# Kernel optimization log

Measured on AMD Instinct MI355X. Metric: run time of the kernel, lower is better.

## Reference

```python
import jax, jax.numpy as jnp
import numpy as np
import math

B = 200        # graphs
NPG = 512      # nodes per graph
EPG = 8192     # edges per graph (avg degree 16)
E = B * EPG
FIN = 11
H = 128


def setup_inputs() -> dict:
    key = jax.random.key(0)
    ks = jax.random.split(key, 16)
    g = jnp.arange(E, dtype=jnp.int32) // EPG  # graph id per edge
    edge_src = g * NPG + jax.random.randint(ks[0], (E,), 0, NPG, dtype=jnp.int32)
    edge_dst = g * NPG + jax.random.randint(ks[1], (E,), 0, NPG, dtype=jnp.int32)
    x = jax.random.normal(ks[2], (B * NPG, FIN), dtype=jnp.float32)

    def w(k, shape):
        return jax.random.normal(k, shape, dtype=jnp.float32) * 0.1

    return dict(
        x=x, edge_src=edge_src, edge_dst=edge_dst,
        num_graphs=B, nodes_per_graph=NPG,
        Wrel1=w(ks[3], (H, FIN)), Wroot1=w(ks[4], (H, FIN)), b1=jnp.zeros((H,), jnp.float32), pw1=w(ks[5], (H,)),
        Wrel2=w(ks[6], (H, H)), Wroot2=w(ks[7], (H, H)), b2=jnp.zeros((H,), jnp.float32), pw2=w(ks[8], (H,)),
        Wrel3=w(ks[9], (H, H)), Wroot3=w(ks[10], (H, H)), b3=jnp.zeros((H,), jnp.float32), pw3=w(ks[11], (H,)),
        Wl1=w(ks[12], (512, 256)), bl1=jnp.zeros((512,), jnp.float32),
        Wl2=w(ks[13], (64, 512)), bl2=jnp.zeros((64,), jnp.float32),
        Wl3=w(ks[14], (1, 64)), bl3=jnp.zeros((1,), jnp.float32),
    )


def graph_conv(x, src, dst, emask, Wrel, Wroot, b):
    # PyG GraphConv (aggr='add'): lin_rel(sum_j x_j) + lin_root(x)
    msg = x[src] * emask[:, None]                    # [E, F] gather + edge mask
    agg = jax.ops.segment_sum(msg, dst, num_segments=x.shape[0])
    return agg @ Wrel.T + b + x @ Wroot.T


def topk_pool(x, src, dst, emask, w, ratio, B):
    # PyG TopKPooling: score = tanh((x . w)/||w||), keep top ceil(ratio*N) per graph
    N = x.shape[0] // B
    k = int(math.ceil(ratio * N))
    score = jnp.tanh((x @ w) / jnp.linalg.norm(w))   # [B*N]
    _, idx = jax.lax.top_k(score.reshape(B, N), k)   # local indices per graph
    perm = (idx + (jnp.arange(B, dtype=idx.dtype) * N)[:, None]).reshape(-1)  # [B*k]
    xk = x[perm] * score[perm][:, None]
    # old node id -> new node id (or -1 if dropped); reindex edges, mask invalid
    newid = jnp.full((B * N,), -1, dtype=jnp.int32).at[perm].set(jnp.arange(B * k, dtype=jnp.int32))
    ns, nd = newid[src], newid[dst]
    keep = emask * (ns >= 0) * (nd >= 0)
    return xk, jnp.maximum(ns, 0), jnp.maximum(nd, 0), keep.astype(x.dtype)


def readout(x, B):
    # cat([global_max_pool, global_mean_pool]); uniform graph sizes -> reshape
    xr = x.reshape(B, -1, x.shape[-1])
    return jnp.concatenate([xr.max(axis=1), xr.mean(axis=1)], axis=-1)


def reference(x, edge_src, edge_dst, num_graphs, nodes_per_graph,
              Wrel1, Wroot1, b1, pw1, Wrel2, Wroot2, b2, pw2,
              Wrel3, Wroot3, b3, pw3, Wl1, bl1, Wl2, bl2, Wl3, bl3):
    Bg = num_graphs
    src, dst = edge_src, edge_dst
    emask = jnp.ones(src.shape, x.dtype)
    h = jax.nn.relu(graph_conv(x, src, dst, emask, Wrel1, Wroot1, b1))
    h, src, dst, emask = topk_pool(h, src, dst, emask, pw1, 0.5, Bg)
    x1 = readout(h, Bg)
    h = jax.nn.relu(graph_conv(h, src, dst, emask, Wrel2, Wroot2, b2))
    h, src, dst, emask = topk_pool(h, src, dst, emask, pw2, 0.8, Bg)
    x2 = readout(h, Bg)
    h = jax.nn.relu(graph_conv(h, src, dst, emask, Wrel3, Wroot3, b3))
    h, src, dst, emask = topk_pool(h, src, dst, emask, pw3, 0.8, Bg)
    x3 = readout(h, Bg)
    z = x1 + x2 + x3
    z = jax.nn.relu(z @ Wl1.T + bl1)   # dropout p=0.7 is identity in eval mode
    z = jax.nn.relu(z @ Wl2.T + bl2)
    return z @ Wl3.T + bl3             # [B, 1]
```

## Files before the change

kernel.cpp:

```cpp
#include <hip/hip_runtime.h>
#include <math.h>

#define BG   200
#define NPGc 512
#define EPGc 8192
#define NE   (BG*EPGc)
#define N0   (BG*NPGc)
#define FINc 11
#define Hc   128
#define K1c  256
#define K2c  205
#define K3c  164
#define N1   (BG*K1c)
#define N2   (BG*K2c)
#define N3   (BG*K3c)

typedef float f32x4 __attribute__((ext_vector_type(4)));
typedef short s16x8 __attribute__((ext_vector_type(8)));

#define PL ((size_t)N1*Hc)
#define PA ((size_t)N0*32)

__device__ inline unsigned short bf16_rne(float v){
  unsigned u = __float_as_uint(v);
  unsigned r = u + 0x7FFFu + ((u >> 16) & 1u);
  return (unsigned short)(r >> 16);
}
__device__ inline float bf16_f32(unsigned short h){
  return __uint_as_float(((unsigned)h) << 16);
}
__device__ inline void split3(float v, unsigned short& r0, unsigned short& r1,
                              unsigned short& r2){
  r0 = bf16_rne(v); float v1 = v - bf16_f32(r0);
  r1 = bf16_rne(v1); float v2 = v1 - bf16_f32(r1);
  r2 = bf16_rne(v2);
}

__device__ inline size_t flIdx(int row, int k){
  return ((size_t)(row >> 4))*2048 + (size_t)(k >> 3)*128
       + (size_t)(row & 15)*8 + (size_t)(k & 7);
}
__device__ inline size_t flIdx32(int row, int k){
  return ((size_t)(row >> 4))*512 + (size_t)(k >> 3)*128
       + (size_t)(row & 15)*8 + (size_t)(k & 7);
}

__launch_bounds__(512)
__global__ void k_csr(const int* __restrict__ esrc, const int* __restrict__ edst,
                      int* __restrict__ deg, int* __restrict__ rowptr,
                      int* __restrict__ csr){
  __shared__ int ed[EPGc];
  __shared__ int cnt[NPGc];
  __shared__ int sc[NPGc];
  int g = blockIdx.x, t = threadIdx.x;
  cnt[t] = 0;
  __syncthreads();
  int gb = g*EPGc;
  for (int i=t; i<EPGc; i+=512){
    int dl = edst[gb+i] & (NPGc-1);
    ed[i] = dl;
    atomicAdd(&cnt[dl], 1);
  }
  __syncthreads();
  int d = cnt[t];
  sc[t] = d;
  __syncthreads();
  for (int o=1;o<NPGc;o<<=1){
    int v = (t>=o) ? sc[t-o] : 0;
    __syncthreads();
    sc[t] += v;
    __syncthreads();
  }
  deg[g*NPGc+t]    = d;
  rowptr[g*NPGc+t] = gb + sc[t] - d;
  cnt[t] = sc[t] - d;
  __syncthreads();
  for (int i=t; i<EPGc; i+=512){
    int p = atomicAdd(&cnt[ed[i]], 1);
    csr[gb+p] = esrc[gb+i];
  }
}

__global__ void k_prepall(const float* __restrict__ Wrel1, const float* __restrict__ Wroot1,
                          const float* __restrict__ Wrel2, const float* __restrict__ Wroot2,
                          const float* __restrict__ Wrel3, const float* __restrict__ Wroot3,
                          const float* __restrict__ Wl1, const float* __restrict__ Wl2,
                          const float* __restrict__ pw1, const float* __restrict__ pw2,
                          const float* __restrict__ pw3,
                          float* __restrict__ Wl1T, float* __restrict__ Wl2T,
                          unsigned short* __restrict__ Wsp, unsigned short* __restrict__ W1S,
                          float* __restrict__ z, float* __restrict__ norms){
  int idx = blockIdx.x*256 + threadIdx.x;
  if (idx < 256*512){
    int f = idx >> 9, t = idx & 511;
    Wl1T[idx] = Wl1[t*256 + f];
  }
  if (idx < 512*64){
    int f = idx >> 6, t = idx & 63;
    Wl2T[idx] = Wl2[t*512 + f];
  }
  if (idx < 65536){
    int L = idx >> 15, p = (idx >> 14) & 1, ck = idx & 16383;
    int c = ck >> 7, k = ck & 127;
    const float* W = L ? (p ? Wroot3 : Wrel3) : (p ? Wroot2 : Wrel2);
    unsigned short r0, r1, r2;
    split3(W[c*128 + k], r0, r1, r2);
    unsigned short* base = Wsp + (size_t)((L*2+p)*3)*16384;
    size_t fl = flIdx(c, k);
    base[fl]          = r0;
    base[16384 + fl]  = r1;
    base[32768 + fl]  = r2;
  }
  if (idx < 4096){
    int c = idx >> 5, k = idx & 31;
    float v = (k < 11) ? Wrel1[c*11 + k] : (k < 22 ? Wroot1[c*11 + (k-11)] : 0.f);
    unsigned short r0, r1, r2;
    split3(v, r0, r1, r2);
    size_t fl = flIdx32(c, k);
    W1S[fl]        = r0;
    W1S[4096 + fl] = r1;
    W1S[8192 + fl] = r2;
  }
  if (idx < BG*256) z[idx] = 0.f;
  if (blockIdx.x == 511){
    int w = threadIdx.x >> 6, lane = threadIdx.x & 63;
    if (w < 3){
      const float* pw = (w==0) ? pw1 : (w==1 ? pw2 : pw3);
      float v0 = pw[lane], v1 = pw[64+lane];
      float ss = v0*v0 + v1*v1;
      for (int o=32;o>0;o>>=1) ss += __shfl_xor(ss, o);
      if (lane == 0) norms[w] = sqrtf(ss);
    }
  }
}

__global__ void k_agg1s(const float* __restrict__ x, const int* __restrict__ csr,
                        const int* __restrict__ rowptr, const int* __restrict__ deg,
                        unsigned short* __restrict__ AS){
  int bid = (int)((blockIdx.x & 7)*3200 + (blockIdx.x >> 3));
  int d = bid*4 + (threadIdx.x >> 6);
  if (d >= N0) return;
  int lane = threadIdx.x & 63;
  int slot = lane >> 4, f = lane & 15;
  int rs = rowptr[d], dg = deg[d];
  float a0 = 0.f, a1 = 0.f;
  for (int base=0; base<dg; base+=64){
    int e = base + lane;
    int s = 0;
    if (e < dg) s = csr[rs+e];
    int cnt = min(64, dg-base);
    for (int jj=0; jj<cnt; jj+=8){
      int s0 = __shfl(s, (jj + slot) & 63);
      int s1 = __shfl(s, (jj + 4 + slot) & 63);
      if (jj + slot < cnt && f < FINc)     a0 += x[s0*FINc + f];
      if (jj + 4 + slot < cnt && f < FINc) a1 += x[s1*FINc + f];
    }
  }
  a0 += a1;
  a0 += __shfl_xor(a0, 16);
  a0 += __shfl_xor(a0, 32);
  int k0 = 2*lane, k1 = k0 + 1;
  float s0 = __shfl(a0, k0 & 15);
  float s1 = __shfl(a0, k1 & 15);
  if (lane < 16){
    float v0 = (k0 < 11) ? s0 : ((k0 < 22) ? x[d*FINc + k0 - 11] : 0.f);
    float v1 = (k1 < 11) ? s1 : ((k1 < 22) ? x[d*FINc + k1 - 11] : 0.f);
    unsigned short a_0,a_1,a_2,b_0,b_1,b_2;
    split3(v0, a_0, a_1, a_2);
    split3(v1, b_0, b_1, b_2);
    size_t fl = flIdx32(d, k0);
    *(unsigned*)&AS[fl]        = (unsigned)a_0 | ((unsigned)b_0 << 16);
    *(unsigned*)&AS[PA + fl]   = (unsigned)a_1 | ((unsigned)b_1 << 16);
    *(unsigned*)&AS[2*PA + fl] = (unsigned)a_2 | ((unsigned)b_2 << 16);
  }
}

__launch_bounds__(256)
__global__ void k_conv1m(const unsigned short* __restrict__ AS,
                         const unsigned short* __restrict__ W1S,
                         const float* __restrict__ bias, const float* __restrict__ pw,
                         const float* __restrict__ norm_p,
                         float* __restrict__ hout, float* __restrict__ score, int M){
  __shared__ float scds[64][2];
  int tid = threadIdx.x;
  int w = tid >> 6, l = tid & 63;
  int wm = w >> 1, wn = w & 1;
  int lr = l & 15, lk = l >> 4;
  int m0 = blockIdx.x * 64;

  f32x4 acc[2][4];
  #pragma unroll
  for (int mi=0;mi<2;mi++)
    #pragma unroll
    for (int ni=0;ni<4;ni++) acc[mi][ni] = (f32x4){0.f,0.f,0.f,0.f};

  s16x8 af[3][2], bf[3][4];
  #pragma unroll
  for (int mi=0; mi<2; mi++){
    int tile = (m0 + wm*32 + mi*16) >> 4;
    size_t idx = (size_t)tile*512 + (size_t)lk*128 + (size_t)lr*8;
    af[0][mi] = *(const s16x8*)&AS[idx];
    af[1][mi] = *(const s16x8*)&AS[PA + idx];
    af[2][mi] = *(const s16x8*)&AS[2*PA + idx];
  }
  #pragma unroll
  for (int ni=0; ni<4; ni++){
    int ct = wn*4 + ni;
    size_t idx = (size_t)ct*512 + (size_t)lk*128 + (size_t)lr*8;
    bf[0][ni] = *(const s16x8*)&W1S[idx];
    bf[1][ni] = *(const s16x8*)&W1S[4096 + idx];
    bf[2][ni] = *(const s16x8*)&W1S[8192 + idx];
  }
  #define TRM(sa,sb) \
    _Pragma("unroll") \
    for (int ni=0; ni<4; ni++){ \
      _Pragma("unroll") \
      for (int mi=0; mi<2; mi++){ \
        acc[mi][ni] = __builtin_amdgcn_mfma_f32_16x16x32_bf16(af[sa][mi], bf[sb][ni], acc[mi][ni], 0,0,0); \
      } \
    }
  TRM(0,0) TRM(0,1) TRM(1,0) TRM(1,1) TRM(0,2) TRM(2,0)
  #undef TRM

  float nrm = *norm_p;
  float pwv[4], biasv[4];
  #pragma unroll
  for (int ni=0;ni<4;ni++){
    int col = wn*64 + ni*16 + lr;
    pwv[ni] = pw[col]; biasv[ni] = bias[col];
  }
  #pragma unroll
  for (int mi=0; mi<2; mi++){
    #pragma unroll
    for (int reg=0; reg<4; reg++){
      int rl = wm*32 + mi*16 + lk*4 + reg;
      int row = m0 + rl;
      float hv[4]; float sc = 0.f;
      #pragma unroll
      for (int ni=0; ni<4; ni++){
        hv[ni] = fmaxf(acc[mi][ni][reg] + biasv[ni], 0.f);
        sc += hv[ni]*pwv[ni];
      }
      if (row < M){
        #pragma unroll
        for (int ni=0; ni<4; ni++)
          hout[(size_t)row*Hc + wn*64 + ni*16 + lr] = hv[ni];
      }
      sc += __shfl_xor(sc,1); sc += __shfl_xor(sc,2);
      sc += __shfl_xor(sc,4); sc += __shfl_xor(sc,8);
      if (lr == 0) scds[rl][wn] = sc;
    }
  }
  __syncthreads();
  if (tid < 64){
    int row = m0 + tid;
    if (row < M) score[row] = tanhf((scds[tid][0] + scds[tid][1]) / nrm);
  }
}

template<int N, int K, int NP2>
__global__ void k_topk(const float* __restrict__ score, int* __restrict__ newid,
                       int* __restrict__ perm,
                       const int* __restrict__ map1In, int* __restrict__ map2Out,
                       const int* __restrict__ origPrev, int* __restrict__ origOut){
  __shared__ float sv[NP2];
  __shared__ int   si[NP2];
  __shared__ int   nid[N];
  int g = blockIdx.x, t = threadIdx.x;
  sv[t] = (t < N) ? score[g*N + t] : -INFINITY;
  si[t] = t;
  __syncthreads();
  for (int k=2;k<=NP2;k<<=1){
    for (int j=k>>1;j>0;j>>=1){
      int p = t ^ j;
      if (p > t){
        float va = sv[t], vb = sv[p];
        int   ia = si[t], ib = si[p];
        bool good = (va > vb) || (va == vb && ia < ib);
        bool up   = ((t & k) == 0);
        if (good != up){ sv[t]=vb; si[t]=ib; sv[p]=va; si[p]=ia; }
      }
      __syncthreads();
    }
  }
  if (t < N) nid[si[t]] = (t < K) ? t : -1;
  __syncthreads();
  if (t < N) newid[g*N + t] = (nid[t] >= 0) ? g*K + nid[t] : -1;
  if (t < K){
    int old = si[t];
    perm[g*K + t] = g*N + old;
    if (origOut) origOut[g*K + t] = origPrev[g*N + old];
  }
  if (map2Out){
    for (int o = t; o < NPGc; o += NP2){
      int m = map1In[g*NPGc + o];
      int r = (m >= 0) ? nid[m - g*N] : -1;
      map2Out[g*NPGc + o] = (r >= 0) ? g*K + r : -1;
    }
  }
}

__launch_bounds__(1024)
__global__ void k_gatherR(const float* __restrict__ h, const float* __restrict__ score,
                          const int* __restrict__ perm, float* __restrict__ hp,
                          unsigned short* __restrict__ hpS, float* __restrict__ z,
                          int kk, int doSplit){
  __shared__ float smx[8][Hc];
  __shared__ float ssm[8][Hc];
  int g = blockIdx.x;
  int rg = threadIdx.x >> 7, j = threadIdx.x & 127;
  float mx = -INFINITY, sm = 0.f;
  for (int r=rg; r<kk; r+=8){
    int m = g*kk + r;
    int p = perm[m];
    float v = h[(size_t)p*Hc + j] * score[p];
    if (hp) hp[(size_t)m*Hc + j] = v;
    float vn = __shfl_xor(v, 1);
    if (doSplit && !(j & 1)){
      unsigned short a0,a1,a2,b0,b1,b2;
      split3(v,  a0, a1, a2);
      split3(vn, b0, b1, b2);
      size_t fl = flIdx(m, j);
      *(unsigned*)&hpS[fl]        = (unsigned)a0 | ((unsigned)b0 << 16);
      *(unsigned*)&hpS[PL + fl]   = (unsigned)a1 | ((unsigned)b1 << 16);
      *(unsigned*)&hpS[2*PL + fl] = (unsigned)a2 | ((unsigned)b2 << 16);
    }
    mx = fmaxf(mx, v); sm += v;
  }
  smx[rg][j] = mx; ssm[rg][j] = sm;
  __syncthreads();
  if (rg == 0){
    #pragma unroll
    for (int u=1; u<8; u++){
      mx = fmaxf(mx, smx[u][j]); sm += ssm[u][j];
    }
    z[g*256 + j]       += mx;
    z[g*256 + 128 + j] += sm / (float)kk;
  }
}

__global__ void k_aggHs(const int* __restrict__ orig, const int* __restrict__ map,
                        const float* __restrict__ hp,
                        const int* __restrict__ csr, const int* __restrict__ rowptr,
                        const int* __restrict__ deg, unsigned short* __restrict__ aggS,
                        int M){
  int cpx = gridDim.x >> 3;
  int bid = (int)((blockIdx.x & 7)*cpx + (blockIdx.x >> 3));
  int m = bid*4 + (threadIdx.x>>6);
  int lane = threadIdx.x & 63;
  if (m >= M) return;
  int d = orig[m];
  int rs = rowptr[d], dg = deg[d];
  int half = lane >> 5, cl = lane & 31;
  f32x4 acc[4];
  #pragma unroll
  for (int u=0;u<4;u++) acc[u] = (f32x4){0.f,0.f,0.f,0.f};
  for (int base=0; base<dg; base+=64){
    int e = base + lane;
    int ns = -1;
    if (e < dg){ int s = csr[rs+e]; ns = map[s]; }
    int cnt = min(64, dg-base);
    for (int jj=0; jj<cnt; jj+=8){
      #pragma unroll
      for (int u=0; u<4; u++){
        int ei = jj + u*2 + half;
        int nsj = __shfl(ns, ei & 63);
        if (ei < cnt && nsj >= 0){
          acc[u] += *(const f32x4*)(hp + (size_t)nsj*Hc + cl*4);
        }
      }
    }
  }
  f32x4 s4 = (acc[0]+acc[1]) + (acc[2]+acc[3]);
  #pragma unroll
  for (int i=0;i<4;i++) s4[i] += __shfl_xor(s4[i], 32);
  float e0 = __shfl(s4[0], lane>>1);
  float e1 = __shfl(s4[1], lane>>1);
  float e2 = __shfl(s4[2], lane>>1);
  float e3 = __shfl(s4[3], lane>>1);
  float cx = (lane&1) ? e2 : e0;
  float cy = (lane&1) ? e3 : e1;
  unsigned short x0,x1,x2,y0,y1,y2;
  split3(cx, x0, x1, x2);
  split3(cy, y0, y1, y2);
  size_t fl = flIdx(m, 2*lane);
  *(unsigned*)&aggS[fl]        = (unsigned)x0 | ((unsigned)y0 << 16);
  *(unsigned*)&aggS[PL + fl]   = (unsigned)x1 | ((unsigned)y1 << 16);
  *(unsigned*)&aggS[2*PL + fl] = (unsigned)x2 | ((unsigned)y2 << 16);
}

__launch_bounds__(256)
__global__ void k_convH(const unsigned short* __restrict__ A0s,
                        const unsigned short* __restrict__ A1s,
                        const unsigned short* __restrict__ Wsp,
                        const float* __restrict__ bias, const float* __restrict__ pw,
                        const float* __restrict__ norm_p,
                        float* __restrict__ hout, float* __restrict__ score, int M){
  __shared__ float scds[64][2];
  int tid = threadIdx.x;
  int w = tid >> 6, l = tid & 63;
  int wm = w >> 1, wn = w & 1;
  int lr = l & 15, lk = l >> 4;
  int m0 = blockIdx.x * 64;

  f32x4 acc[2][4];
  #pragma unroll
  for (int mi=0;mi<2;mi++)
    #pragma unroll
    for (int ni=0;ni<4;ni++) acc[mi][ni] = (f32x4){0.f,0.f,0.f,0.f};

  #pragma unroll
  for (int kc=0; kc<4; kc++){
    #pragma unroll
    for (int p=0; p<2; p++){
      const unsigned short* As = p ? A1s : A0s;
      const unsigned short* Wp = Wsp + (size_t)p*3*16384;
      s16x8 af[3][2], bf[3][4];
      #pragma unroll
      for (int mi=0; mi<2; mi++){
        int tile = (m0 + wm*32 + mi*16) >> 4;
        size_t idx = (size_t)tile*2048 + (size_t)(kc*4+lk)*128 + (size_t)lr*8;
        af[0][mi] = *(const s16x8*)&As[idx];
        af[1][mi] = *(const s16x8*)&As[PL + idx];
        af[2][mi] = *(const s16x8*)&As[2*PL + idx];
      }
      #pragma unroll
      for (int ni=0; ni<4; ni++){
        int ct = wn*4 + ni;
        size_t idx = (size_t)ct*2048 + (size_t)(kc*4+lk)*128 + (size_t)lr*8;
        bf[0][ni] = *(const s16x8*)&Wp[idx];
        bf[1][ni] = *(const s16x8*)&Wp[16384 + idx];
        bf[2][ni] = *(const s16x8*)&Wp[32768 + idx];
      }
      #define TRM(sa,sb) \
        _Pragma("unroll") \
        for (int ni=0; ni<4; ni++){ \
          _Pragma("unroll") \
          for (int mi=0; mi<2; mi++){ \
            acc[mi][ni] = __builtin_amdgcn_mfma_f32_16x16x32_bf16(af[sa][mi], bf[sb][ni], acc[mi][ni], 0,0,0); \
          } \
        }
      TRM(0,0) TRM(0,1) TRM(1,0) TRM(1,1) TRM(0,2) TRM(2,0)
      #undef TRM
    }
  }

  float nrm = *norm_p;
  float pwv[4], biasv[4];
  #pragma unroll
  for (int ni=0;ni<4;ni++){
    int col = wn*64 + ni*16 + lr;
    pwv[ni] = pw[col]; biasv[ni] = bias[col];
  }
  #pragma unroll
  for (int mi=0; mi<2; mi++){
    #pragma unroll
    for (int reg=0; reg<4; reg++){
      int rl = wm*32 + mi*16 + lk*4 + reg;
      int row = m0 + rl;
      float hv[4]; float sc = 0.f;
      #pragma unroll
      for (int ni=0; ni<4; ni++){
        hv[ni] = fmaxf(acc[mi][ni][reg] + biasv[ni], 0.f);
        sc += hv[ni]*pwv[ni];
      }
      if (row < M){
        #pragma unroll
        for (int ni=0; ni<4; ni++)
          hout[(size_t)row*Hc + wn*64 + ni*16 + lr] = hv[ni];
      }
      sc += __shfl_xor(sc,1); sc += __shfl_xor(sc,2);
      sc += __shfl_xor(sc,4); sc += __shfl_xor(sc,8);
      if (lr == 0) scds[rl][wn] = sc;
    }
  }
  __syncthreads();
  if (tid < 64){
    int row = m0 + tid;
    if (row < M) score[row] = tanhf((scds[tid][0] + scds[tid][1]) / nrm);
  }
}

__launch_bounds__(512)
__global__ void k_mlp(const float* __restrict__ z,
                      const float* __restrict__ Wl1T, const float* __restrict__ bl1,
                      const float* __restrict__ Wl2T, const float* __restrict__ bl2,
                      const float* __restrict__ Wl3, const float* __restrict__ bl3,
                      float* __restrict__ out){
  __shared__ float zs[256];
  __shared__ float u1[512];
  int g = blockIdx.x, t = threadIdx.x;
  if (t < 256) zs[t] = z[g*256 + t];
  __syncthreads();
  {
    float acc = bl1[t];
    #pragma unroll 8
    for (int f=0; f<256; f++) acc = fmaf(zs[f], Wl1T[f*512 + t], acc);
    u1[t] = fmaxf(acc, 0.f);
  }
  __syncthreads();
  if (t < 64){
    float acc = bl2[t];
    #pragma unroll 8
    for (int f=0; f<512; f++) acc = fmaf(u1[f], Wl2T[f*64 + t], acc);
    float v = fmaxf(acc, 0.f) * Wl3[t];
    for (int o=32;o>0;o>>=1) v += __shfl_xor(v, o);
    if (t == 0) out[g] = v + bl3[0];
  }
}

extern "C" void kernel_launch(void* const* d_in, const int* in_sizes, int n_in,
                              void* d_out, int out_size, void* d_ws, size_t ws_size,
                              hipStream_t stream){
  const float* x     = (const float*)d_in[0];
  const int*   esrc  = (const int*)d_in[1];
  const int*   edst  = (const int*)d_in[2];
  const float* Wrel1 = (const float*)d_in[5];
  const float* Wroot1= (const float*)d_in[6];
  const float* b1    = (const float*)d_in[7];
  const float* pw1   = (const float*)d_in[8];
  const float* Wrel2 = (const float*)d_in[9];
  const float* Wroot2= (const float*)d_in[10];
  const float* b2    = (const float*)d_in[11];
  const float* pw2   = (const float*)d_in[12];
  const float* Wrel3 = (const float*)d_in[13];
  const float* Wroot3= (const float*)d_in[14];
  const float* b3    = (const float*)d_in[15];
  const float* pw3   = (const float*)d_in[16];
  const float* Wl1   = (const float*)d_in[17];
  const float* bl1   = (const float*)d_in[18];
  const float* Wl2   = (const float*)d_in[19];
  const float* bl2   = (const float*)d_in[20];
  const float* Wl3   = (const float*)d_in[21];
  const float* bl3   = (const float*)d_in[22];
  float* out = (float*)d_out;

  char* ws = (char*)d_ws;
  size_t off = 0;
  auto alloc = [&](size_t elems)->void*{
    void* p = ws + off;
    off += ((elems*4 + 255)/256)*256;
    return p;
  };
  int*   deg    = (int*)alloc(N0);
  int*   rowptr = (int*)alloc(N0);
  int*   csr    = (int*)alloc(NE);
  int*   map1   = (int*)alloc(N0);
  int*   newid2 = (int*)alloc(N1);
  int*   map2   = (int*)alloc(N0);
  int*   perm1  = (int*)alloc(N1);
  int*   perm2  = (int*)alloc(N2);
  int*   perm3  = (int*)alloc(N3);
  int*   orig3  = (int*)alloc(N2);
  float* score1 = (float*)alloc(N0);
  float* score2 = (float*)alloc(N1);
  float* score3 = (float*)alloc(N2);
  float* Wl1T   = (float*)alloc(256*512);
  float* Wl2T   = (float*)alloc(512*64);
  unsigned short* Wsp = (unsigned short*)alloc(98304);
  unsigned short* W1S = (unsigned short*)alloc(6144);
  float* norms  = (float*)alloc(3);
  float* bigA   = (float*)alloc((size_t)N0*Hc);
  float* hB     = (float*)alloc((size_t)N1*Hc);
  float* hpA    = (float*)alloc((size_t)N1*Hc);
  unsigned short* hpS = (unsigned short*)alloc((size_t)3*N1*Hc/2);
  float* z      = (float*)alloc(BG*256);

  float* h1   = bigA;
  unsigned short* aggS = (unsigned short*)bigA;
  unsigned short* a1S  = hpS;
  float* h2   = hB;
  float* h3   = hB;

  k_prepall<<<512, 256, 0, stream>>>(Wrel1, Wroot1, Wrel2, Wroot2, Wrel3, Wroot3,
                                     Wl1, Wl2, pw1, pw2, pw3,
                                     Wl1T, Wl2T, Wsp, W1S, z, norms);
  k_csr    <<<BG, 512, 0, stream>>>(esrc, edst, deg, rowptr, csr);

  k_agg1s  <<<N0/4, 256, 0, stream>>>(x, csr, rowptr, deg, a1S);
  k_conv1m <<<N0/64, 256, 0, stream>>>(a1S, W1S, b1, pw1, norms+0, h1, score1, N0);
  k_topk<NPGc, K1c, 512><<<BG, 512, 0, stream>>>(score1, map1, perm1,
                                                 nullptr, nullptr, nullptr, nullptr);
  k_gatherR<<<BG, 1024, 0, stream>>>(h1, score1, perm1, hpA, hpS, z, K1c, 1);

  k_aggHs  <<<N1/4, 256, 0, stream>>>(perm1, map1, hpA, csr, rowptr, deg, aggS, N1);
  k_convH  <<<N1/64, 256, 0, stream>>>(aggS, hpS, Wsp, b2, pw2, norms+1, h2, score2, N1);
  k_topk<K1c, K2c, 256><<<BG, 256, 0, stream>>>(score2, newid2, perm2,
                                                map1, map2, perm1, orig3);
  k_gatherR<<<BG, 1024, 0, stream>>>(h2, score2, perm2, hpA, hpS, z, K2c, 1);

  k_aggHs  <<<10256, 256, 0, stream>>>(orig3, map2, hpA, csr, rowptr, deg, aggS, N2);
  k_convH  <<<(N2+63)/64, 256, 0, stream>>>(aggS, hpS, Wsp + 98304, b3, pw3, norms+2,
                                            h3, score3, N2);
  k_topk<K2c, K3c, 256><<<BG, 256, 0, stream>>>(score3, newid2, perm3,
                                                nullptr, nullptr, nullptr, nullptr);
  k_gatherR<<<BG, 1024, 0, stream>>>(h3, score3, perm3, nullptr, nullptr, z, K3c, 0);

  k_mlp<<<BG, 512, 0, stream>>>(z, Wl1T, bl1, Wl2T, bl2, Wl3, bl3, out);
}
```

Measured before the change: 313.8 us.

## Merge CSR build and weight prep into one launch, pad x, unroll aggregation

Fuses the CSR construction and weight-preparation kernels into a single block-partitioned front kernel. The same kernel also writes a 16-float padded copy of the node features, so the layer-1 aggregation uses aligned shift-indexed loads without feature-bound checks. Separately, the hidden-layer aggregation unrolls over 16 edges with 8 accumulators to keep more gathers in flight. The trade-offs are an extra padded feature buffer and higher register pressure in the aggregation kernel.

Result: no change. 310.7 us (-1.0%).

```diff
diff --git a/kernel.cpp b/kernel.cpp
--- a/kernel.cpp
+++ b/kernel.cpp
@@ -46,95 +46,102 @@
 }
 
 __launch_bounds__(512)
-__global__ void k_csr(const int* __restrict__ esrc, const int* __restrict__ edst,
-                      int* __restrict__ deg, int* __restrict__ rowptr,
-                      int* __restrict__ csr){
-  __shared__ int ed[EPGc];
-  __shared__ int cnt[NPGc];
-  __shared__ int sc[NPGc];
-  int g = blockIdx.x, t = threadIdx.x;
-  cnt[t] = 0;
-  __syncthreads();
-  int gb = g*EPGc;
-  for (int i=t; i<EPGc; i+=512){
-    int dl = edst[gb+i] & (NPGc-1);
-    ed[i] = dl;
-    atomicAdd(&cnt[dl], 1);
-  }
-  __syncthreads();
-  int d = cnt[t];
-  sc[t] = d;
-  __syncthreads();
-  for (int o=1;o<NPGc;o<<=1){
-    int v = (t>=o) ? sc[t-o] : 0;
+__global__ void k_front(const int* __restrict__ esrc, const int* __restrict__ edst,
+                        const float* __restrict__ x,
+                        const float* __restrict__ Wrel1, const float* __restrict__ Wroot1,
+                        const float* __restrict__ Wrel2, const float* __restrict__ Wroot2,
+                        const float* __restrict__ Wrel3, const float* __restrict__ Wroot3,
+                        const float* __restrict__ Wl1, const float* __restrict__ Wl2,
+                        const float* __restrict__ pw1, const float* __restrict__ pw2,
+                        const float* __restrict__ pw3,
+                        int* __restrict__ deg, int* __restrict__ rowptr,
+                        int* __restrict__ csr, float* __restrict__ xp,
+                        float* __restrict__ Wl1T, float* __restrict__ Wl2T,
+                        unsigned short* __restrict__ Wsp, unsigned short* __restrict__ W1S,
+                        float* __restrict__ z, float* __restrict__ norms){
+  int b = blockIdx.x, t = threadIdx.x;
+  if (b < BG){
+    __shared__ int ed[EPGc];
+    __shared__ int cnt[NPGc];
+    __shared__ int sc[NPGc];
+    int g = b;
+    cnt[t] = 0;
     __syncthreads();
-    sc[t] += v;
+    int gb = g*EPGc;
+    for (int i=t; i<EPGc; i+=512){
+      int dl = edst[gb+i] & (NPGc-1);
+      ed[i] = dl;
+      atomicAdd(&cnt[dl], 1);
+    }
     __syncthreads();
-  }
-  deg[g*NPGc+t]    = d;
-  rowptr[g*NPGc+t] = gb + sc[t] - d;
-  cnt[t] = sc[t] - d;
-  __syncthreads();
-  for (int i=t; i<EPGc; i+=512){
-    int p = atomicAdd(&cnt[ed[i]], 1);
-    csr[gb+p] = esrc[gb+i];
-  }
-}
-
-__global__ void k_prepall(const float* __restrict__ Wrel1, const float* __restrict__ Wroot1,
-                          const float* __restrict__ Wrel2, const float* __restrict__ Wroot2,
-                          const float* __restrict__ Wrel3, const float* __restrict__ Wroot3,
-                          const float* __restrict__ Wl1, const float* __restrict__ Wl2,
-                          const float* __restrict__ pw1, const float* __restrict__ pw2,
-                          const float* __restrict__ pw3,
-                          float* __restrict__ Wl1T, float* __restrict__ Wl2T,
-                          unsigned short* __restrict__ Wsp, unsigned short* __restrict__ W1S,
-                          float* __restrict__ z, float* __restrict__ norms){
-  int idx = blockIdx.x*256 + threadIdx.x;
-  if (idx < 256*512){
-    int f = idx >> 9, t = idx & 511;
-    Wl1T[idx] = Wl1[t*256 + f];
-  }
-  if (idx < 512*64){
-    int f = idx >> 6, t = idx & 63;
-    Wl2T[idx] = Wl2[t*512 + f];
-  }
-  if (idx < 65536){
-    int L = idx >> 15, p = (idx >> 14) & 1, ck = idx & 16383;
-    int c = ck >> 7, k = ck & 127;
-    const float* W = L ? (p ? Wroot3 : Wrel3) : (p ? Wroot2 : Wrel2);
-    unsigned short r0, r1, r2;
-    split3(W[c*128 + k], r0, r1, r2);
-    unsigned short* base = Wsp + (size_t)((L*2+p)*3)*16384;
-    size_t fl = flIdx(c, k);
-    base[fl]          = r0;
-    base[16384 + fl]  = r1;
-    base[32768 + fl]  = r2;
-  }
-  if (idx < 4096){
-    int c = idx >> 5, k = idx & 31;
-    float v = (k < 11) ? Wrel1[c*11 + k] : (k < 22 ? Wroot1[c*11 + (k-11)] : 0.f);
-    unsigned short r0, r1, r2;
-    split3(v, r0, r1, r2);
-    size_t fl = flIdx32(c, k);
-    W1S[fl]        = r0;
-    W1S[4096 + fl] = r1;
-    W1S[8192 + fl] = r2;
-  }
-  if (idx < BG*256) z[idx] = 0.f;
-  if (blockIdx.x == 511){
-    int w = threadIdx.x >> 6, lane = threadIdx.x & 63;
-    if (w < 3){
-      const float* pw = (w==0) ? pw1 : (w==1 ? pw2 : pw3);
-      float v0 = pw[lane], v1 = pw[64+lane];
-      float ss = v0*v0 + v1*v1;
-      for (int o=32;o>0;o>>=1) ss += __shfl_xor(ss, o);
-      if (lane == 0) norms[w] = sqrtf(ss);
-    }
-  }
-}
-
-__global__ void k_agg1s(const float* __restrict__ x, const int* __restrict__ csr,
+    int d = cnt[t];
+    sc[t] = d;
+    __syncthreads();
+    for (int o=1;o<NPGc;o<<=1){
+      int v = (t>=o) ? sc[t-o] : 0;
+      __syncthreads();
+      sc[t] += v;
+      __syncthreads();
+    }
+    deg[g*NPGc+t]    = d;
+    rowptr[g*NPGc+t] = gb + sc[t] - d;
+    cnt[t] = sc[t] - d;
+    __syncthreads();
+    for (int i=t; i<EPGc; i+=512){
+      int p = atomicAdd(&cnt[ed[i]], 1);
+      csr[gb+p] = esrc[gb+i];
+    }
+  } else if (b < 456){
+    int idx = (b-200)*512 + t;
+    if (idx < 256*512){
+      int f = idx >> 9, tt = idx & 511;
+      Wl1T[idx] = Wl1[tt*256 + f];
+    }
+    if (idx < 512*64){
+      int f = idx >> 6, tt = idx & 63;
+      Wl2T[idx] = Wl2[tt*512 + f];
+    }
+    if (idx < 65536){
+      int L = idx >> 15, p = (idx >> 14) & 1, ck = idx & 16383;
+      int c = ck >> 7, k = ck & 127;
+      const float* W = L ? (p ? Wroot3 : Wrel3) : (p ? Wroot2 : Wrel2);
+      unsigned short r0, r1, r2;
+      split3(W[c*128 + k], r0, r1, r2);
+      unsigned short* base = Wsp + (size_t)((L*2+p)*3)*16384;
+      size_t fl = flIdx(c, k);
+      base[fl]          = r0;
+      base[16384 + fl]  = r1;
+      base[32768 + fl]  = r2;
+    }
+    if (idx < 4096){
+      int c = idx >> 5, k = idx & 31;
+      float v = (k < 11) ? Wrel1[c*11 + k] : (k < 22 ? Wroot1[c*11 + (k-11)] : 0.f);
+      unsigned short r0, r1, r2;
+      split3(v, r0, r1, r2);
+      size_t fl = flIdx32(c, k);
+      W1S[fl]        = r0;
+      W1S[4096 + fl] = r1;
+      W1S[8192 + fl] = r2;
+    }
+    if (idx < BG*256) z[idx] = 0.f;
+    if (b == 455){
+      int w = t >> 6, lane = t & 63;
+      if (w < 3){
+        const float* pw = (w==0) ? pw1 : (w==1 ? pw2 : pw3);
+        float v0 = pw[lane], v1 = pw[64+lane];
+        float ss = v0*v0 + v1*v1;
+        for (int o=32;o>0;o>>=1) ss += __shfl_xor(ss, o);
+        if (lane == 0) norms[w] = sqrtf(ss);
+      }
+    }
+  } else {
+    int idx = (b-456)*512 + t;
+    int n = idx >> 4, f = idx & 15;
+    xp[idx] = (f < FINc) ? x[n*FINc + f] : 0.f;
+  }
+}
+
+__global__ void k_agg1s(const float* __restrict__ xp, const int* __restrict__ csr,
                         const int* __restrict__ rowptr, const int* __restrict__ deg,
                         unsigned short* __restrict__ AS){
   int bid = (int)((blockIdx.x & 7)*3200 + (blockIdx.x >> 3));
@@ -152,8 +159,8 @@
     for (int jj=0; jj<cnt; jj+=8){
       int s0 = __shfl(s, (jj + slot) & 63);
       int s1 = __shfl(s, (jj + 4 + slot) & 63);
-      if (jj + slot < cnt && f < FINc)     a0 += x[s0*FINc + f];
-      if (jj + 4 + slot < cnt && f < FINc) a1 += x[s1*FINc + f];
+      if (jj + slot < cnt)     a0 += xp[(s0<<4) + f];
+      if (jj + 4 + slot < cnt) a1 += xp[(s1<<4) + f];
     }
   }
   a0 += a1;
@@ -163,8 +170,8 @@
   float s0 = __shfl(a0, k0 & 15);
   float s1 = __shfl(a0, k1 & 15);
   if (lane < 16){
-    float v0 = (k0 < 11) ? s0 : ((k0 < 22) ? x[d*FINc + k0 - 11] : 0.f);
-    float v1 = (k1 < 11) ? s1 : ((k1 < 22) ? x[d*FINc + k1 - 11] : 0.f);
+    float v0 = (k0 < 11) ? s0 : ((k0 < 22) ? xp[(d<<4) + k0 - 11] : 0.f);
+    float v1 = (k1 < 11) ? s1 : ((k1 < 22) ? xp[(d<<4) + k1 - 11] : 0.f);
     unsigned short a_0,a_1,a_2,b_0,b_1,b_2;
     split3(v0, a_0, a_1, a_2);
     split3(v1, b_0, b_1, b_2);
@@ -352,17 +359,17 @@
   int d = orig[m];
   int rs = rowptr[d], dg = deg[d];
   int half = lane >> 5, cl = lane & 31;
-  f32x4 acc[4];
-  #pragma unroll
-  for (int u=0;u<4;u++) acc[u] = (f32x4){0.f,0.f,0.f,0.f};
+  f32x4 acc[8];
+  #pragma unroll
+  for (int u=0;u<8;u++) acc[u] = (f32x4){0.f,0.f,0.f,0.f};
   for (int base=0; base<dg; base+=64){
     int e = base + lane;
     int ns = -1;
     if (e < dg){ int s = csr[rs+e]; ns = map[s]; }
     int cnt = min(64, dg-base);
-    for (int jj=0; jj<cnt; jj+=8){
+    for (int jj=0; jj<cnt; jj+=16){
       #pragma unroll
-      for (int u=0; u<4; u++){
+      for (int u=0; u<8; u++){
         int ei = jj + u*2 + half;
         int nsj = __shfl(ns, ei & 63);
         if (ei < cnt && nsj >= 0){
@@ -371,7 +378,7 @@
       }
     }
   }
-  f32x4 s4 = (acc[0]+acc[1]) + (acc[2]+acc[3]);
+  f32x4 s4 = ((acc[0]+acc[1]) + (acc[2]+acc[3])) + ((acc[4]+acc[5]) + (acc[6]+acc[7]));
   #pragma unroll
   for (int i=0;i<4;i++) s4[i] += __shfl_xor(s4[i], 32);
   float e0 = __shfl(s4[0], lane>>1);
@@ -555,6 +562,7 @@
   float* score1 = (float*)alloc(N0);
   float* score2 = (float*)alloc(N1);
   float* score3 = (float*)alloc(N2);
+  float* xp     = (float*)alloc((size_t)N0*16);
   float* Wl1T   = (float*)alloc(256*512);
   float* Wl2T   = (float*)alloc(512*64);
   unsigned short* Wsp = (unsigned short*)alloc(98304);
@@ -572,12 +580,13 @@
   float* h2   = hB;
   float* h3   = hB;
 
-  k_prepall<<<512, 256, 0, stream>>>(Wrel1, Wroot1, Wrel2, Wroot2, Wrel3, Wroot3,
-                                     Wl1, Wl2, pw1, pw2, pw3,
-                                     Wl1T, Wl2T, Wsp, W1S, z, norms);
-  k_csr    <<<BG, 512, 0, stream>>>(esrc, edst, deg, rowptr, csr);
-
-  k_agg1s  <<<N0/4, 256, 0, stream>>>(x, csr, rowptr, deg, a1S);
+  k_front<<<3656, 512, 0, stream>>>(esrc, edst, x,
+                                    Wrel1, Wroot1, Wrel2, Wroot2, Wrel3, Wroot3,
+                                    Wl1, Wl2, pw1, pw2, pw3,
+                                    deg, rowptr, csr, xp,
+                                    Wl1T, Wl2T, Wsp, W1S, z, norms);
+
+  k_agg1s  <<<N0/4, 256, 0, stream>>>(xp, csr, rowptr, deg, a1S);
   k_conv1m <<<N0/64, 256, 0, stream>>>(a1S, W1S, b1, pw1, norms+0, h1, score1, N0);
   k_topk<NPGc, K1c, 512><<<BG, 512, 0, stream>>>(score1, map1, perm1,
                                                  nullptr, nullptr, nullptr, nullptr);
```
